# Kernel optimization log

Hardware: AMD Instinct MI355X
Metric: run time of the kernel (lower is better)

The kernel has to match this reference:

```python
import jax, jax.numpy as jnp
import numpy as np

N = 50000      # nodes
D_IN = 128     # input_dim
D_OUT = 128    # output_dim
K = 4          # number of core adjacencies (len(adj_list))
E = 600000     # edges per adjacency
LN_EPS = 1e-5


def setup_inputs() -> dict:
    key = jax.random.key(0)
    ks = jax.random.split(key, 9)
    x = jax.random.normal(ks[0], (N, D_IN), dtype=jnp.float32)
    rows = jax.random.randint(ks[1], (K, E), 0, N, dtype=jnp.int32)
    cols = jax.random.randint(ks[2], (K, E), 0, N, dtype=jnp.int32)
    vals = jax.random.uniform(ks[3], (K, E), dtype=jnp.float32)
    std = 1.0 / np.sqrt(D_OUT)  # GRUCell.reset_parameters uniform(-std, std)
    w_x = jax.random.uniform(ks[4], (3 * D_OUT, D_IN), jnp.float32, -std, std)
    b_x = jax.random.uniform(ks[5], (3 * D_OUT,), jnp.float32, -std, std)
    w_h = jax.random.uniform(ks[6], (3 * D_OUT, D_OUT), jnp.float32, -std, std)
    b_h = jax.random.uniform(ks[7], (3 * D_OUT,), jnp.float32, -std, std)
    ln_g = jnp.ones((D_OUT,), jnp.float32)
    ln_b = jnp.zeros((D_OUT,), jnp.float32)
    return {"x": x, "vals": vals, "w_x": w_x, "b_x": b_x, "w_h": w_h,
            "b_h": b_h, "ln_g": ln_g, "ln_b": ln_b, "rows": rows, "cols": cols}


def reference(x, vals, w_x, b_x, w_h, b_h, ln_g, ln_b, rows, cols):
    n = x.shape[0]

    def step(h, inp):
        r, c, v = inp  # COO sparse adj for this diffusion step
        # torch.sparse.mm(adj, x): gather source rows, scale, scatter-add to dest
        msg = v[:, None] * x[c]                              # [E, D_IN]
        res = jax.nn.relu(jax.ops.segment_sum(msg, r, num_segments=n))
        # GRUCell
        gate_x = res @ w_x.T + b_x                           # [N, 3*D_OUT]
        gate_h = h @ w_h.T + b_h
        i_r, i_i, i_n = jnp.split(gate_x, 3, axis=1)
        h_r, h_i, h_n = jnp.split(gate_h, 3, axis=1)
        resetgate = jax.nn.sigmoid(i_r + h_r)
        inputgate = jax.nn.sigmoid(i_i + h_i)
        newgate = jnp.tanh(i_n + resetgate * h_n)
        hy = newgate + inputgate * (h - newgate)
        return hy, None

    # adj_list = adj_list[::-1]
    h0 = jnp.zeros((n, D_OUT), dtype=x.dtype)
    h, _ = jax.lax.scan(step, h0, (rows[::-1], cols[::-1], vals[::-1]))
    # LayerNorm(output_dim)
    mean = jnp.mean(h, axis=-1, keepdims=True)
    var = jnp.var(h, axis=-1, keepdims=True)
    return (h - mean) / jnp.sqrt(var + LN_EPS) * ln_g + ln_b
```

## Files before the change

kernel.cpp:

```cpp
#include <hip/hip_runtime.h>
#include <cstdint>

#define NN 50000
#define DD 128
#define EE 600000
#define NBK 49
#define BCAP 14336

typedef __attribute__((ext_vector_type(8))) short bf16x8;
typedef __attribute__((ext_vector_type(4))) float f32x4;

__device__ __forceinline__ float sigmoid_f(float x) {
    return 1.0f / (1.0f + __expf(-x));
}
__device__ __forceinline__ float tanh_f(float x) {
    float e = __expf(-2.0f * fabsf(x));
    float t = (1.0f - e) / (1.0f + e);
    return copysignf(t, x);
}
__device__ __forceinline__ unsigned short bf16_rn(float v) {
    unsigned u = __float_as_uint(v);
    u = u + 0x7fffu + ((u >> 16) & 1u);
    return (unsigned short)(u >> 16);
}
__device__ __forceinline__ float bf16_tf(unsigned short h) {
    return __uint_as_float(((unsigned)h) << 16);
}

__global__ __launch_bounds__(256) void pack_w_kernel(const float* __restrict__ wx,
                                                     const float* __restrict__ wh,
                                                     unsigned short* __restrict__ Wp) {
    int idx = blockIdx.x * 256 + threadIdx.x;
    if (idx >= 24 * 512 * 32) return;
    int k8 = idx & 31;
    int n = (idx >> 5) & 511;
    int kb = idx >> 14;
    int grp = kb >> 2;
    int k = (kb & 3) * 32 + k8;
    float v = 0.f;
    if (grp < 3) {
        if (n < 384) v = wx[n * 128 + k];
    } else {
        if (n < 256) v = wh[n * 128 + k];
        else if (n >= 384) v = wh[(n - 128) * 128 + k];
    }
    unsigned short hi = bf16_rn(v);
    bool lo = (grp == 2) || (grp == 5);
    Wp[idx] = lo ? bf16_rn(v - bf16_tf(hi)) : hi;
}


__global__ __launch_bounds__(256) void bhist_kernel(const int* __restrict__ rows,
                                                    int* __restrict__ bcnt4) {
    __shared__ int lc[NBK];
    const int tid = threadIdx.x;
    const int k = blockIdx.y;
    const int e0 = blockIdx.x * 2048;
    if (tid < NBK) lc[tid] = 0;
    __syncthreads();
    #pragma unroll
    for (int i = 0; i < 8; ++i) {
        int e = e0 + i * 256 + tid;
        if (e < EE) atomicAdd(&lc[rows[(size_t)k * EE + e] >> 10], 1);
    }
    __syncthreads();
    if (tid < NBK && lc[tid]) atomicAdd(&bcnt4[k * NBK + tid], lc[tid]);
}

__global__ __launch_bounds__(64) void bscan_kernel(const int* __restrict__ bcnt4,
                                                   int* __restrict__ bbase4,
                                                   int* __restrict__ bcur4) {
    int k = threadIdx.x;
    if (k < 4) {
        int run = 0;
        for (int b = 0; b < NBK; ++b) {
            bbase4[k * NBK + b] = run;
            bcur4[k * NBK + b] = run;
            run += bcnt4[k * NBK + b];
        }
    }
}

__global__ __launch_bounds__(256) void bscat_kernel(const int* __restrict__ rows,
                                                    const int* __restrict__ cols,
                                                    const float* __restrict__ vals,
                                                    int* __restrict__ bcur4,
                                                    int2* __restrict__ st2) {
    __shared__ int lcnt[4][NBK];
    __shared__ int sstart4[4][NBK];
    __shared__ int sstart_b[NBK];
    __shared__ int gbase[NBK];
    __shared__ int ltot;
    __shared__ int sw0[2048];
    __shared__ int sw1[2048];
    __shared__ unsigned char sbk[2048];

    const int tid = threadIdx.x;
    const int w = tid >> 6;
    const int k = blockIdx.y;
    const int e0 = blockIdx.x * 2048;

    if (tid < NBK) { lcnt[0][tid] = 0; lcnt[1][tid] = 0; lcnt[2][tid] = 0; lcnt[3][tid] = 0; }
    __syncthreads();

    int eb[8], er[8], ew0[8], ew1[8];
    #pragma unroll
    for (int i = 0; i < 8; ++i) {
        int e = e0 + i * 256 + tid;
        eb[i] = -1;
        if (e < EE) {
            size_t off = (size_t)k * EE + e;
            int r = rows[off];
            int b = r >> 10;
            eb[i] = b;
            er[i] = atomicAdd(&lcnt[w][b], 1);
            ew0[i] = ((r & 1023) << 17) | cols[off];
            ew1[i] = __float_as_int(vals[off]);
        }
    }
    __syncthreads();
    if (tid == 0) {
        int run = 0;
        for (int b = 0; b < NBK; ++b) {
            sstart_b[b] = run;
            #pragma unroll
            for (int q = 0; q < 4; ++q) { sstart4[q][b] = run; run += lcnt[q][b]; }
        }
        ltot = run;
    }
    __syncthreads();
    if (tid < NBK) {
        int n = (sstart4[3][tid] + lcnt[3][tid]) - sstart_b[tid];
        if (n) gbase[tid] = atomicAdd(&bcur4[k * NBK + tid], n);
    }
    __syncthreads();
    #pragma unroll
    for (int i = 0; i < 8; ++i) {
        if (eb[i] >= 0) {
            int slot = sstart4[w][eb[i]] + er[i];
            sw0[slot] = ew0[i];
            sw1[slot] = ew1[i];
            sbk[slot] = (unsigned char)eb[i];
        }
    }
    __syncthreads();
    const int tot = ltot;
    #pragma unroll
    for (int i = 0; i < 8; ++i) {
        int slot = i * 256 + tid;
        if (slot < tot) {
            int b = sbk[slot];
            int pos = gbase[b] + (slot - sstart_b[b]);
            st2[(size_t)k * EE + pos] = make_int2(sw0[slot], sw1[slot]);
        }
    }
}

__global__ __launch_bounds__(1024, 1) void sort2_kernel(const int2* __restrict__ st2,
                                                        const int* __restrict__ bbase4,
                                                        const int* __restrict__ bcnt4,
                                                        int* __restrict__ row_ptr4,
                                                        int2* __restrict__ epair4) {
    __shared__ int cnt[1024];
    __shared__ int cur[1024];
    __shared__ int2 obuf[BCAP];

    const int tid = threadIdx.x;
    const int b = blockIdx.x;
    const int k = blockIdx.y;
    const int base = bbase4[k * NBK + b];
    const int n = bcnt4[k * NBK + b];

    cnt[tid] = 0;
    __syncthreads();
    for (int i = tid; i < n; i += 1024)
        atomicAdd(&cnt[st2[(size_t)k * EE + base + i].x >> 17], 1);
    __syncthreads();

    int v = cnt[tid];
    cur[tid] = v;
    __syncthreads();
    for (int d = 1; d < 1024; d <<= 1) {
        int t = (tid >= d) ? cur[tid - d] : 0;
        __syncthreads();
        cur[tid] += t;
        __syncthreads();
    }
    int excl = cur[tid] - v;

    int grow = b * 1024 + tid;
    if (grow <= NN) row_ptr4[k * (NN + 1) + grow] = base + excl;

    cur[tid] = excl;
    __syncthreads();
    for (int i = tid; i < n; i += 1024) {
        int2 p = st2[(size_t)k * EE + base + i];
        int rl = p.x >> 17;
        int pos = atomicAdd(&cur[rl], 1);
        if (pos < BCAP) obuf[pos] = make_int2(p.x & 0x1FFFF, p.y);
    }
    __syncthreads();
    for (int i = tid; i < n; i += 1024)
        epair4[(size_t)k * EE + base + i] = obuf[i];
}

__global__ __launch_bounds__(256) void gather_kernel(const float* __restrict__ x,
                                                     const int* __restrict__ row_ptr,
                                                     const int2* __restrict__ epair,
                                                     unsigned short* __restrict__ Rh,
                                                     unsigned short* __restrict__ Rl) {
    const int tid = threadIdx.x;
    const int row = blockIdx.x * 8 + (tid >> 5);
    const int d0 = (tid & 31) * 4;
    const int start = row_ptr[row];
    const int end = row_ptr[row + 1];
    float4 a0 = make_float4(0.f, 0.f, 0.f, 0.f);
    float4 a1 = a0, a2 = a0, a3 = a0;
    int e = start;
    for (; e + 3 < end; e += 4) {
        int2 p0 = epair[e], p1 = epair[e + 1], p2 = epair[e + 2], p3 = epair[e + 3];
        float4 x0 = *reinterpret_cast<const float4*>(x + (size_t)p0.x * DD + d0);
        float4 x1 = *reinterpret_cast<const float4*>(x + (size_t)p1.x * DD + d0);
        float4 x2 = *reinterpret_cast<const float4*>(x + (size_t)p2.x * DD + d0);
        float4 x3 = *reinterpret_cast<const float4*>(x + (size_t)p3.x * DD + d0);
        float v0 = __int_as_float(p0.y), v1 = __int_as_float(p1.y);
        float v2 = __int_as_float(p2.y), v3 = __int_as_float(p3.y);
        a0.x += v0 * x0.x; a0.y += v0 * x0.y; a0.z += v0 * x0.z; a0.w += v0 * x0.w;
        a1.x += v1 * x1.x; a1.y += v1 * x1.y; a1.z += v1 * x1.z; a1.w += v1 * x1.w;
        a2.x += v2 * x2.x; a2.y += v2 * x2.y; a2.z += v2 * x2.z; a2.w += v2 * x2.w;
        a3.x += v3 * x3.x; a3.y += v3 * x3.y; a3.z += v3 * x3.z; a3.w += v3 * x3.w;
    }
    for (; e < end; ++e) {
        int2 p0 = epair[e];
        float v0 = __int_as_float(p0.y);
        float4 x0 = *reinterpret_cast<const float4*>(x + (size_t)p0.x * DD + d0);
        a0.x += v0 * x0.x; a0.y += v0 * x0.y; a0.z += v0 * x0.z; a0.w += v0 * x0.w;
    }
    float o[4];
    o[0] = fmaxf((a0.x + a1.x) + (a2.x + a3.x), 0.f);
    o[1] = fmaxf((a0.y + a1.y) + (a2.y + a3.y), 0.f);
    o[2] = fmaxf((a0.z + a1.z) + (a2.z + a3.z), 0.f);
    o[3] = fmaxf((a0.w + a1.w) + (a2.w + a3.w), 0.f);
    ushort4 vh, vl;
    unsigned short h0 = bf16_rn(o[0]); vh.x = h0; vl.x = bf16_rn(o[0] - bf16_tf(h0));
    unsigned short h1 = bf16_rn(o[1]); vh.y = h1; vl.y = bf16_rn(o[1] - bf16_tf(h1));
    unsigned short h2 = bf16_rn(o[2]); vh.z = h2; vl.z = bf16_rn(o[2] - bf16_tf(h2));
    unsigned short h3 = bf16_rn(o[3]); vh.w = h3; vl.w = bf16_rn(o[3] - bf16_tf(h3));
    *reinterpret_cast<ushort4*>(Rh + (size_t)row * DD + d0) = vh;
    *reinterpret_cast<ushort4*>(Rl + (size_t)row * DD + d0) = vl;
}

template <bool FIRST, bool LAST>
__global__ __launch_bounds__(512, 4)
void gemm_gru_kernel(const unsigned short* __restrict__ Rh,
                     const unsigned short* __restrict__ Rl,
                     unsigned int* __restrict__ Hpk,
                     float* __restrict__ hout,
                     const unsigned short* __restrict__ Wp,
                     const float* __restrict__ bx,
                     const float* __restrict__ bh) {
    __shared__ unsigned short sA[2 * 64 * 128];

    const int tid = threadIdx.x;
    const int row0 = blockIdx.x * 64;
    const int lane = tid & 63;
    const int w = tid >> 6;
    const int g = lane >> 4;
    const int m16 = lane & 15;

    f32x4 acc[4][4];
    #pragma unroll
    for (int G = 0; G < 4; ++G)
        #pragma unroll
        for (int mt = 0; mt < 4; ++mt)
            acc[G][mt] = (f32x4){0.f, 0.f, 0.f, 0.f};

    auto stageA = [&]() {
        #pragma unroll
        for (int it = 0; it < 4; ++it) {
            int arr = it >> 1;
            int idx = (it & 1) * 512 + tid;
            int row = idx >> 4;
            int slot = idx & 15;
            int grow = row0 + row;
            uint4 v = make_uint4(0, 0, 0, 0);
            if (grow < NN) {
                const unsigned short* src = arr ? Rl : Rh;
                v = *reinterpret_cast<const uint4*>(src + (size_t)grow * 128 + slot * 8);
            }
            int sw = slot ^ (row & 7);
            *reinterpret_cast<uint4*>(sA + ((arr * 64 + row) * 16 + sw) * 8) = v;
        }
    };

    auto stageH = [&]() {
        #pragma unroll
        for (int it = 0; it < 4; ++it) {
            int idx = it * 512 + tid;
            int row = idx >> 5;
            int j0 = (idx & 31) * 4;
            int grow = row0 + row;
            uint4 v = make_uint4(0, 0, 0, 0);
            if (grow < NN)
                v = *reinterpret_cast<const uint4*>(Hpk + (size_t)grow * 128 + j0);
            ushort4 hh = make_ushort4(v.x & 0xFFFF, v.y & 0xFFFF, v.z & 0xFFFF, v.w & 0xFFFF);
            ushort4 hl = make_ushort4(v.x >> 16, v.y >> 16, v.z >> 16, v.w >> 16);
            int sw = (j0 >> 3) ^ (row & 7);
            int b0 = ((0 * 64 + row) * 16 + sw) * 8 + (j0 & 7);
            int b1 = ((1 * 64 + row) * 16 + sw) * 8 + (j0 & 7);
            *reinterpret_cast<ushort4*>(sA + b0) = hh;
            *reinterpret_cast<ushort4*>(sA + b1) = hl;
        }
    };

    auto do_kb2 = [&](int kbW, int kq, int arr, int G0, int G1, int G2) {
        bf16x8 bfr[3];
        const int Gs[3] = {G0, G1, G2};
        #pragma unroll
        for (int i = 0; i < 3; ++i) {
            int n = Gs[i] * 128 + w * 16 + m16;
            bfr[i] = *reinterpret_cast<const bf16x8*>(
                Wp + ((size_t)(kbW * 512 + n)) * 32 + g * 8);
        }
        bf16x8 afr[4];
        #pragma unroll
        for (int mt = 0; mt < 4; ++mt) {
            int row = mt * 16 + m16;
            int sw = (kq * 4 + g) ^ (row & 7);
            afr[mt] = *reinterpret_cast<const bf16x8*>(
                sA + ((arr * 64 + row) * 16 + sw) * 8);
        }
        __builtin_amdgcn_s_setprio(1);
        #pragma unroll
        for (int mt = 0; mt < 4; ++mt) {
            acc[G0][mt] = __builtin_amdgcn_mfma_f32_16x16x32_bf16(afr[mt], bfr[0], acc[G0][mt], 0, 0, 0);
            acc[G1][mt] = __builtin_amdgcn_mfma_f32_16x16x32_bf16(afr[mt], bfr[1], acc[G1][mt], 0, 0, 0);
            acc[G2][mt] = __builtin_amdgcn_mfma_f32_16x16x32_bf16(afr[mt], bfr[2], acc[G2][mt], 0, 0, 0);
        }
        __builtin_amdgcn_s_setprio(0);
    };

    stageA();
    __syncthreads();
    for (int kq = 0; kq < 4; ++kq) {
        do_kb2(kq,     kq, 0, 0, 1, 2);
        do_kb2(kq,     kq, 1, 0, 1, 2);
        do_kb2(8 + kq, kq, 0, 0, 1, 2);
    }

    if (!FIRST) {
        __syncthreads();
        stageH();
        __syncthreads();
        for (int kq = 0; kq < 4; ++kq) {
            do_kb2(12 + kq, kq, 0, 0, 1, 3);
            do_kb2(12 + kq, kq, 1, 0, 1, 3);
            do_kb2(20 + kq, kq, 0, 0, 1, 3);
        }
    }

    {
        int j = w * 16 + m16;
        float bxr = bx[j], bxi = bx[128 + j], bxn = bx[256 + j];
        float bhr = bh[j], bhi = bh[128 + j], bhn = bh[256 + j];
        #pragma unroll
        for (int mt = 0; mt < 4; ++mt) {
            #pragma unroll
            for (int ii = 0; ii < 4; ++ii) {
                int lrow = mt * 16 + g * 4 + ii;
                int grow = row0 + lrow;
                if (grow >= NN) continue;
                float rr = acc[0][mt][ii] + bxr + bhr;
                float ri = acc[1][mt][ii] + bxi + bhi;
                float rin = acc[2][mt][ii] + bxn;
                float rhn = bhn;
                float ho = 0.f;
                if (!FIRST) {
                    rhn += acc[3][mt][ii];
                    int sw = (j >> 3) ^ (lrow & 7);
                    int bi = (lrow * 16 + sw) * 8 + (j & 7);
                    ho = bf16_tf(sA[bi]) + bf16_tf(sA[64 * 128 + bi]);
                }
                float rg = sigmoid_f(rr);
                float ig = sigmoid_f(ri);
                float ng = tanh_f(rin + rg * rhn);
                float hy = ng + ig * (ho - ng);
                if (LAST) {
                    hout[(size_t)grow * 128 + j] = hy;
                } else {
                    unsigned short hh = bf16_rn(hy);
                    unsigned short hl = bf16_rn(hy - bf16_tf(hh));
                    Hpk[(size_t)grow * 128 + j] = (unsigned)hh | ((unsigned)hl << 16);
                }
            }
        }
    }
}

__global__ __launch_bounds__(256) void ln_kernel(float* __restrict__ h,
                                                 const float* __restrict__ g,
                                                 const float* __restrict__ b) {
    int tid = threadIdx.x;
    int lane = tid & 31;
    int rl = tid >> 5;
    int row = blockIdx.x * 8 + rl;
    if (row >= NN) return;
    float4 v = *reinterpret_cast<const float4*>(h + (size_t)row * DD + lane * 4);
    float s = v.x + v.y + v.z + v.w;
    #pragma unroll
    for (int m = 16; m >= 1; m >>= 1) s += __shfl_xor(s, m, 64);
    float mean = s * (1.0f / DD);
    float dx = v.x - mean, dy = v.y - mean, dz = v.z - mean, dw = v.w - mean;
    float q = dx * dx + dy * dy + dz * dz + dw * dw;
    #pragma unroll
    for (int m = 16; m >= 1; m >>= 1) q += __shfl_xor(q, m, 64);
    float var = q * (1.0f / DD);
    float inv = 1.0f / sqrtf(var + 1e-5f);
    float4 gv = *reinterpret_cast<const float4*>(g + lane * 4);
    float4 bv = *reinterpret_cast<const float4*>(b + lane * 4);
    float4 o;
    o.x = dx * inv * gv.x + bv.x;
    o.y = dy * inv * gv.y + bv.y;
    o.z = dz * inv * gv.z + bv.z;
    o.w = dw * inv * gv.w + bv.w;
    *reinterpret_cast<float4*>(h + (size_t)row * DD + lane * 4) = o;
}

static inline size_t align_up(size_t v, size_t a) { return (v + a - 1) & ~(a - 1); }

extern "C" void kernel_launch(void* const* d_in, const int* in_sizes, int n_in,
                              void* d_out, int out_size, void* d_ws, size_t ws_size,
                              hipStream_t stream) {
    const float* x    = (const float*)d_in[0];
    const float* vals = (const float*)d_in[1];
    const float* wx   = (const float*)d_in[2];
    const float* bx   = (const float*)d_in[3];
    const float* wh   = (const float*)d_in[4];
    const float* bh   = (const float*)d_in[5];
    const float* lng  = (const float*)d_in[6];
    const float* lnb  = (const float*)d_in[7];
    const int* rows   = (const int*)d_in[8];
    const int* cols   = (const int*)d_in[9];

    float* hout = (float*)d_out;

    size_t off = 0;
    char* wsb = (char*)d_ws;
    unsigned short* Rh = (unsigned short*)(wsb + off); off = align_up(off + (size_t)NN * DD * 2, 256);
    unsigned short* Rl = (unsigned short*)(wsb + off); off = align_up(off + (size_t)NN * DD * 2, 256);
    unsigned int* Hpk = (unsigned int*)(wsb + off);    off = align_up(off + (size_t)NN * DD * 4, 256);
    unsigned short* Wp = (unsigned short*)(wsb + off); off = align_up(off + (size_t)24 * 512 * 32 * 2, 256);
    int* row_ptr4 = (int*)(wsb + off);  off = align_up(off + (size_t)4 * (NN + 1) * 4, 256);
    int2* epair4 = (int2*)(wsb + off);  off = align_up(off + (size_t)4 * EE * 8, 256);
    int* bcnt4 = (int*)(wsb + off);     off = align_up(off + (size_t)4 * NBK * 4, 256);
    int* bbase4 = (int*)(wsb + off);    off = align_up(off + (size_t)4 * NBK * 4, 256);
    int* bcur4 = (int*)(wsb + off);     off = align_up(off + (size_t)4 * NBK * 4, 256);
    int2* st2 = (int2*)wsb;

    (void)in_sizes; (void)n_in; (void)out_size; (void)ws_size;

    pack_w_kernel<<<1536, 256, 0, stream>>>(wx, wh, Wp);

    hipMemsetAsync(bcnt4, 0, (size_t)4 * NBK * sizeof(int), stream);
    dim3 e2grid((EE + 2047) / 2048, 4);
    bhist_kernel<<<e2grid, 256, 0, stream>>>(rows, bcnt4);
    bscan_kernel<<<1, 64, 0, stream>>>(bcnt4, bbase4, bcur4);
    bscat_kernel<<<e2grid, 256, 0, stream>>>(rows, cols, vals, bcur4, st2);
    dim3 sgrid(NBK, 4);
    sort2_kernel<<<sgrid, 1024, 0, stream>>>(st2, bbase4, bcnt4, row_ptr4, epair4);

    const int ggrid = NN / 8;
    const int mgrid = (NN + 63) / 64;

    for (int s = 0; s < 4; ++s) {
        int k = 3 - s;
        gather_kernel<<<ggrid, 256, 0, stream>>>(
            x, row_ptr4 + (size_t)k * (NN + 1), epair4 + (size_t)k * EE, Rh, Rl);
        if (s == 0)
            gemm_gru_kernel<true, false><<<mgrid, 512, 0, stream>>>(
                Rh, Rl, Hpk, hout, Wp, bx, bh);
        else if (s < 3)
            gemm_gru_kernel<false, false><<<mgrid, 512, 0, stream>>>(
                Rh, Rl, Hpk, hout, Wp, bx, bh);
        else
            gemm_gru_kernel<false, true><<<mgrid, 512, 0, stream>>>(
                Rh, Rl, Hpk, hout, Wp, bx, bh);
    }

    ln_kernel<<<(NN + 7) / 8, 256, 0, stream>>>(hout, lng, lnb);
}
```

Measured before the change: 412.5 us.

## Fuse sparse gather into GEMM-GRU kernel, writing aggregated rows straight to LDS

The separate gather kernel is removed. Each GEMM-GRU block now computes the SpMM aggregation for its own 64 rows and writes the bf16 hi/lo split directly into the swizzled shared-memory A tile. This drops the global Rh/Rl round trip and one kernel launch per step. The gather now runs inside a kernel with launch_bounds(512,4) and heavy register use, so latency hiding for the random x loads may be worse, and the gather cannot overlap with MFMA work. The staging buffer st2 moves to its own workspace region.

```diff
diff --git a/kernel.cpp b/kernel.cpp
--- a/kernel.cpp
+++ b/kernel.cpp
@@ -204,56 +204,11 @@
         epair4[(size_t)k * EE + base + i] = obuf[i];
 }
 
-__global__ __launch_bounds__(256) void gather_kernel(const float* __restrict__ x,
-                                                     const int* __restrict__ row_ptr,
-                                                     const int2* __restrict__ epair,
-                                                     unsigned short* __restrict__ Rh,
-                                                     unsigned short* __restrict__ Rl) {
-    const int tid = threadIdx.x;
-    const int row = blockIdx.x * 8 + (tid >> 5);
-    const int d0 = (tid & 31) * 4;
-    const int start = row_ptr[row];
-    const int end = row_ptr[row + 1];
-    float4 a0 = make_float4(0.f, 0.f, 0.f, 0.f);
-    float4 a1 = a0, a2 = a0, a3 = a0;
-    int e = start;
-    for (; e + 3 < end; e += 4) {
-        int2 p0 = epair[e], p1 = epair[e + 1], p2 = epair[e + 2], p3 = epair[e + 3];
-        float4 x0 = *reinterpret_cast<const float4*>(x + (size_t)p0.x * DD + d0);
-        float4 x1 = *reinterpret_cast<const float4*>(x + (size_t)p1.x * DD + d0);
-        float4 x2 = *reinterpret_cast<const float4*>(x + (size_t)p2.x * DD + d0);
-        float4 x3 = *reinterpret_cast<const float4*>(x + (size_t)p3.x * DD + d0);
-        float v0 = __int_as_float(p0.y), v1 = __int_as_float(p1.y);
-        float v2 = __int_as_float(p2.y), v3 = __int_as_float(p3.y);
-        a0.x += v0 * x0.x; a0.y += v0 * x0.y; a0.z += v0 * x0.z; a0.w += v0 * x0.w;
-        a1.x += v1 * x1.x; a1.y += v1 * x1.y; a1.z += v1 * x1.z; a1.w += v1 * x1.w;
-        a2.x += v2 * x2.x; a2.y += v2 * x2.y; a2.z += v2 * x2.z; a2.w += v2 * x2.w;
-        a3.x += v3 * x3.x; a3.y += v3 * x3.y; a3.z += v3 * x3.z; a3.w += v3 * x3.w;
-    }
-    for (; e < end; ++e) {
-        int2 p0 = epair[e];
-        float v0 = __int_as_float(p0.y);
-        float4 x0 = *reinterpret_cast<const float4*>(x + (size_t)p0.x * DD + d0);
-        a0.x += v0 * x0.x; a0.y += v0 * x0.y; a0.z += v0 * x0.z; a0.w += v0 * x0.w;
-    }
-    float o[4];
-    o[0] = fmaxf((a0.x + a1.x) + (a2.x + a3.x), 0.f);
-    o[1] = fmaxf((a0.y + a1.y) + (a2.y + a3.y), 0.f);
-    o[2] = fmaxf((a0.z + a1.z) + (a2.z + a3.z), 0.f);
-    o[3] = fmaxf((a0.w + a1.w) + (a2.w + a3.w), 0.f);
-    ushort4 vh, vl;
-    unsigned short h0 = bf16_rn(o[0]); vh.x = h0; vl.x = bf16_rn(o[0] - bf16_tf(h0));
-    unsigned short h1 = bf16_rn(o[1]); vh.y = h1; vl.y = bf16_rn(o[1] - bf16_tf(h1));
-    unsigned short h2 = bf16_rn(o[2]); vh.z = h2; vl.z = bf16_rn(o[2] - bf16_tf(h2));
-    unsigned short h3 = bf16_rn(o[3]); vh.w = h3; vl.w = bf16_rn(o[3] - bf16_tf(h3));
-    *reinterpret_cast<ushort4*>(Rh + (size_t)row * DD + d0) = vh;
-    *reinterpret_cast<ushort4*>(Rl + (size_t)row * DD + d0) = vl;
-}
-
 template <bool FIRST, bool LAST>
 __global__ __launch_bounds__(512, 4)
-void gemm_gru_kernel(const unsigned short* __restrict__ Rh,
-                     const unsigned short* __restrict__ Rl,
+void gemm_gru_kernel(const float* __restrict__ x,
+                     const int* __restrict__ row_ptr,
+                     const int2* __restrict__ epair,
                      unsigned int* __restrict__ Hpk,
                      float* __restrict__ hout,
                      const unsigned short* __restrict__ Wp,
@@ -268,30 +223,65 @@
     const int g = lane >> 4;
     const int m16 = lane & 15;
 
+    {
+        const int hw = tid >> 5;
+        const int l32 = tid & 31;
+        const int d0 = l32 * 4;
+        #pragma unroll
+        for (int p = 0; p < 4; ++p) {
+            int rl = p * 16 + hw;
+            int grow = row0 + rl;
+            float4 a0 = make_float4(0.f, 0.f, 0.f, 0.f);
+            float4 a1 = a0, a2 = a0, a3 = a0;
+            if (grow < NN) {
+                int start = row_ptr[grow];
+                int end = row_ptr[grow + 1];
+                int e = start;
+                for (; e + 3 < end; e += 4) {
+                    int2 p0 = epair[e], p1 = epair[e + 1], p2 = epair[e + 2], p3 = epair[e + 3];
+                    float4 x0 = *reinterpret_cast<const float4*>(x + (size_t)p0.x * DD + d0);
+                    float4 x1 = *reinterpret_cast<const float4*>(x + (size_t)p1.x * DD + d0);
+                    float4 x2 = *reinterpret_cast<const float4*>(x + (size_t)p2.x * DD + d0);
+                    float4 x3 = *reinterpret_cast<const float4*>(x + (size_t)p3.x * DD + d0);
+                    float v0 = __int_as_float(p0.y), v1 = __int_as_float(p1.y);
+                    float v2 = __int_as_float(p2.y), v3 = __int_as_float(p3.y);
+                    a0.x += v0 * x0.x; a0.y += v0 * x0.y; a0.z += v0 * x0.z; a0.w += v0 * x0.w;
+                    a1.x += v1 * x1.x; a1.y += v1 * x1.y; a1.z += v1 * x1.z; a1.w += v1 * x1.w;
+                    a2.x += v2 * x2.x; a2.y += v2 * x2.y; a2.z += v2 * x2.z; a2.w += v2 * x2.w;
+                    a3.x += v3 * x3.x; a3.y += v3 * x3.y; a3.z += v3 * x3.z; a3.w += v3 * x3.w;
+                }
+                for (; e < end; ++e) {
+                    int2 p0 = epair[e];
+                    float v0 = __int_as_float(p0.y);
+                    float4 x0 = *reinterpret_cast<const float4*>(x + (size_t)p0.x * DD + d0);
+                    a0.x += v0 * x0.x; a0.y += v0 * x0.y; a0.z += v0 * x0.z; a0.w += v0 * x0.w;
+                }
+            }
+            float o[4];
+            o[0] = fmaxf((a0.x + a1.x) + (a2.x + a3.x), 0.f);
+            o[1] = fmaxf((a0.y + a1.y) + (a2.y + a3.y), 0.f);
+            o[2] = fmaxf((a0.z + a1.z) + (a2.z + a3.z), 0.f);
+            o[3] = fmaxf((a0.w + a1.w) + (a2.w + a3.w), 0.f);
+            ushort4 vh, vl;
+            unsigned short h0 = bf16_rn(o[0]); vh.x = h0; vl.x = bf16_rn(o[0] - bf16_tf(h0));
+            unsigned short h1 = bf16_rn(o[1]); vh.y = h1; vl.y = bf16_rn(o[1] - bf16_tf(h1));
+            unsigned short h2 = bf16_rn(o[2]); vh.z = h2; vl.z = bf16_rn(o[2] - bf16_tf(h2));
+            unsigned short h3 = bf16_rn(o[3]); vh.w = h3; vl.w = bf16_rn(o[3] - bf16_tf(h3));
+            int slot = l32 >> 1;
+            int sw = slot ^ (rl & 7);
+            int bi = ((0 * 64 + rl) * 16 + sw) * 8 + (d0 & 7);
+            *reinterpret_cast<ushort4*>(sA + bi) = vh;
+            *reinterpret_cast<ushort4*>(sA + (64 * 128) + bi) = vl;
+        }
+    }
+    __syncthreads();
+
     f32x4 acc[4][4];
     #pragma unroll
     for (int G = 0; G < 4; ++G)
         #pragma unroll
         for (int mt = 0; mt < 4; ++mt)
             acc[G][mt] = (f32x4){0.f, 0.f, 0.f, 0.f};
-
-    auto stageA = [&]() {
-        #pragma unroll
-        for (int it = 0; it < 4; ++it) {
-            int arr = it >> 1;
-            int idx = (it & 1) * 512 + tid;
-            int row = idx >> 4;
-            int slot = idx & 15;
-            int grow = row0 + row;
-            uint4 v = make_uint4(0, 0, 0, 0);
-            if (grow < NN) {
-                const unsigned short* src = arr ? Rl : Rh;
-                v = *reinterpret_cast<const uint4*>(src + (size_t)grow * 128 + slot * 8);
-            }
-            int sw = slot ^ (row & 7);
-            *reinterpret_cast<uint4*>(sA + ((arr * 64 + row) * 16 + sw) * 8) = v;
-        }
-    };
 
     auto stageH = [&]() {
         #pragma unroll
@@ -340,8 +330,6 @@
         __builtin_amdgcn_s_setprio(0);
     };
 
-    stageA();
-    __syncthreads();
     for (int kq = 0; kq < 4; ++kq) {
         do_kb2(kq,     kq, 0, 0, 1, 2);
         do_kb2(kq,     kq, 1, 0, 1, 2);
@@ -446,8 +434,7 @@
 
     size_t off = 0;
     char* wsb = (char*)d_ws;
-    unsigned short* Rh = (unsigned short*)(wsb + off); off = align_up(off + (size_t)NN * DD * 2, 256);
-    unsigned short* Rl = (unsigned short*)(wsb + off); off = align_up(off + (size_t)NN * DD * 2, 256);
+    int2* st2 = (int2*)(wsb + off);     off = align_up(off + (size_t)4 * EE * 8, 256);
     unsigned int* Hpk = (unsigned int*)(wsb + off);    off = align_up(off + (size_t)NN * DD * 4, 256);
     unsigned short* Wp = (unsigned short*)(wsb + off); off = align_up(off + (size_t)24 * 512 * 32 * 2, 256);
     int* row_ptr4 = (int*)(wsb + off);  off = align_up(off + (size_t)4 * (NN + 1) * 4, 256);
@@ -455,7 +442,6 @@
     int* bcnt4 = (int*)(wsb + off);     off = align_up(off + (size_t)4 * NBK * 4, 256);
     int* bbase4 = (int*)(wsb + off);    off = align_up(off + (size_t)4 * NBK * 4, 256);
     int* bcur4 = (int*)(wsb + off);     off = align_up(off + (size_t)4 * NBK * 4, 256);
-    int2* st2 = (int2*)wsb;
 
     (void)in_sizes; (void)n_in; (void)out_size; (void)ws_size;
 
@@ -469,22 +455,21 @@
     dim3 sgrid(NBK, 4);
     sort2_kernel<<<sgrid, 1024, 0, stream>>>(st2, bbase4, bcnt4, row_ptr4, epair4);
 
-    const int ggrid = NN / 8;
     const int mgrid = (NN + 63) / 64;
 
     for (int s = 0; s < 4; ++s) {
         int k = 3 - s;
-        gather_kernel<<<ggrid, 256, 0, stream>>>(
-            x, row_ptr4 + (size_t)k * (NN + 1), epair4 + (size_t)k * EE, Rh, Rl);
+        const int* rp = row_ptr4 + (size_t)k * (NN + 1);
+        const int2* ep = epair4 + (size_t)k * EE;
         if (s == 0)
             gemm_gru_kernel<true, false><<<mgrid, 512, 0, stream>>>(
-                Rh, Rl, Hpk, hout, Wp, bx, bh);
+                x, rp, ep, Hpk, hout, Wp, bx, bh);
         else if (s < 3)
             gemm_gru_kernel<false, false><<<mgrid, 512, 0, stream>>>(
-                Rh, Rl, Hpk, hout, Wp, bx, bh);
+                x, rp, ep, Hpk, hout, Wp, bx, bh);
         else
             gemm_gru_kernel<false, true><<<mgrid, 512, 0, stream>>>(
-                Rh, Rl, Hpk, hout, Wp, bx, bh);
+                x, rp, ep, Hpk, hout, Wp, bx, bh);
     }
 
     ln_kernel<<<(NN + 7) / 8, 256, 0, stream>>>(hout, lng, lnb);
```

New measurement: 401.7 us, median of 2. -2.6%, faster.
